# Kernel optimization log

Hardware: AMD Instinct MI355X
Metric: run time of the kernel (lower is better)

## Reference

```python
import jax, jax.numpy as jnp
import numpy as np

NUM_HEADS = 8
NUM_GROUPS = 8
EPS = 1e-5


def setup_inputs() -> dict:
    key = jax.random.key(0)
    ks = jax.random.split(key, 4)
    B, C, H, W = 16, 512, 32, 32
    x = jax.random.normal(ks[0], (B, C, H, W), dtype=jnp.float32)
    gamma = jnp.ones((C,), jnp.float32)
    beta = jnp.zeros((C,), jnp.float32)
    w_qkv = jax.random.normal(ks[1], (3 * C, C), jnp.float32) * (1.0 / np.sqrt(C))
    b_qkv = jnp.zeros((3 * C,), jnp.float32)
    w_out = jax.random.normal(ks[2], (C, C), jnp.float32) * (1.0 / np.sqrt(C))
    b_out = jnp.zeros((C,), jnp.float32)
    return {"x": x, "gamma": gamma, "beta": beta, "w_qkv": w_qkv,
            "b_qkv": b_qkv, "w_out": w_out, "b_out": b_out}


def _group_norm(x, gamma, beta):
    b, c, h, w = x.shape
    xg = x.reshape(b, NUM_GROUPS, c // NUM_GROUPS, h, w)
    mean = xg.mean(axis=(2, 3, 4), keepdims=True)
    var = xg.var(axis=(2, 3, 4), keepdims=True)
    xn = ((xg - mean) * jax.lax.rsqrt(var + EPS)).reshape(b, c, h, w)
    return xn * gamma[None, :, None, None] + beta[None, :, None, None]


def reference(x, gamma, beta, w_qkv, b_qkv, w_out, b_out):
    b, c, h, w = x.shape
    hd = c // NUM_HEADS
    scale = hd ** -0.5
    xn = _group_norm(x, gamma, beta)
    # 1x1 conv == per-pixel linear: (3c, c) x (b, c, h, w) -> (b, 3c, h, w)
    qkv = jnp.einsum('oc,bchw->bohw', w_qkv, xn) + b_qkv[None, :, None, None]
    q, k, v = jnp.split(qkv, 3, axis=1)
    q = q.reshape(b, NUM_HEADS, hd, h * w)
    k = k.reshape(b, NUM_HEADS, hd, h * w)
    v = v.reshape(b, NUM_HEADS, hd, h * w)
    attn = jnp.einsum('bhdi,bhdj->bhij', q, k) * scale  # (b, heads, hw, hw)
    attn = jax.nn.softmax(attn, axis=-1)
    out = jnp.einsum('bhij,bhdj->bhdi', attn, v).reshape(b, c, h, w)
    out = jnp.einsum('oc,bchw->bohw', w_out, out) + b_out[None, :, None, None]
    return x + out
```

## Files before the change

### kernel.cpp

```cpp
#include <hip/hip_runtime.h>
#include <hip/hip_bf16.h>

#define BB   16
#define CCH  512
#define PP   1024
#define NHD  8

typedef unsigned short u16;
typedef unsigned int   u32;
typedef __attribute__((ext_vector_type(8))) short bf16x8;
typedef __attribute__((ext_vector_type(4))) float f32x4;

__device__ __forceinline__ float us2f(u16 u) {
    return __uint_as_float(((u32)u) << 16);
}
__device__ __forceinline__ u16 f2bu(float f) {
    __hip_bfloat16 h = __float2bfloat16(f);
    return *reinterpret_cast<u16*>(&h);
}

__launch_bounds__(256)
__global__ void gn_stats_k(const float* __restrict__ x,
                           float* __restrict__ ps, float* __restrict__ pss) {
    int blk = blockIdx.x;
    int bg = blk >> 2, part = blk & 3;
    const float4* xp = (const float4*)(x + (size_t)bg * 65536 + (size_t)part * 16384);
    float s = 0.f, ss = 0.f;
    for (int i = threadIdx.x; i < 4096; i += 256) {
        float4 v = xp[i];
        s  += v.x + v.y + v.z + v.w;
        ss += v.x*v.x + v.y*v.y + v.z*v.z + v.w*v.w;
    }
    __shared__ float sh[256], sq[256];
    sh[threadIdx.x] = s; sq[threadIdx.x] = ss;
    __syncthreads();
    for (int off = 128; off > 0; off >>= 1) {
        if (threadIdx.x < off) {
            sh[threadIdx.x] += sh[threadIdx.x + off];
            sq[threadIdx.x] += sq[threadIdx.x + off];
        }
        __syncthreads();
    }
    if (threadIdx.x == 0) {
        ps[blk]  = sh[0];
        pss[blk] = sq[0];
    }
}

__launch_bounds__(256)
__global__ void conv_x_k(const float* __restrict__ x,
                         const float* __restrict__ ps, const float* __restrict__ pss,
                         const float* __restrict__ gamma, const float* __restrict__ beta,
                         u16* __restrict__ xbt) {
    __shared__ u16 T[64][73];
    const int tid = threadIdx.x;
    const int p0 = blockIdx.x * 64;
    const int c0 = blockIdx.y * 64;
    const int b  = blockIdx.z;
    const int bg = (b << 3) + (c0 >> 6);
    float s4  = ps[bg*4]  + ps[bg*4+1]  + ps[bg*4+2]  + ps[bg*4+3];
    float ss4 = pss[bg*4] + pss[bg*4+1] + pss[bg*4+2] + pss[bg*4+3];
    float m   = s4 * (1.f / 65536.f);
    float var = ss4 * (1.f / 65536.f) - m * m;
    float rs  = rsqrtf(var + 1e-5f);
    {
        int ci = tid >> 2, psx = (tid & 3) * 16;
        int c = c0 + ci;
        float sc = rs * gamma[c];
        float sf = beta[c] - m * sc;
        const float* xp = x + ((size_t)(b * CCH + c)) * PP + p0 + psx;
        #pragma unroll
        for (int j4 = 0; j4 < 4; j4++) {
            float4 v = *(const float4*)(xp + j4 * 4);
            T[psx + j4*4 + 0][ci] = f2bu(v.x * sc + sf);
            T[psx + j4*4 + 1][ci] = f2bu(v.y * sc + sf);
            T[psx + j4*4 + 2][ci] = f2bu(v.z * sc + sf);
            T[psx + j4*4 + 3][ci] = f2bu(v.w * sc + sf);
        }
    }
    __syncthreads();
    {
        int pi = tid >> 2, cs = (tid & 3) * 16;
        u16* dst = xbt + ((size_t)(b * PP) + p0 + pi) * CCH + c0 + cs;
        #pragma unroll
        for (int j4 = 0; j4 < 4; j4++) {
            ushort4 o;
            o.x = T[pi][cs + j4*4 + 0]; o.y = T[pi][cs + j4*4 + 1];
            o.z = T[pi][cs + j4*4 + 2]; o.w = T[pi][cs + j4*4 + 3];
            *(ushort4*)(dst + j4 * 4) = o;
        }
    }
}

__launch_bounds__(256)
__global__ void conv_w_k(const float* __restrict__ w1, const float* __restrict__ w2,
                         u16* __restrict__ d1, u16* __restrict__ d2) {
    int id = blockIdx.x * 256 + threadIdx.x;
    const float* s; u16* d; int off;
    if (id < 196608) { s = w1; d = d1; off = id * 4; }
    else             { s = w2; d = d2; off = (id - 196608) * 4; }
    float4 v = *(const float4*)(s + off);
    ushort4 o;
    o.x = f2bu(v.x); o.y = f2bu(v.y); o.z = f2bu(v.z); o.w = f2bu(v.w);
    *(ushort4*)(d + off) = o;
}

__launch_bounds__(256)
__global__ void mgemm_qkv_k(const u16* __restrict__ Wb, const float* __restrict__ bias,
                            const u16* __restrict__ actT,
                            u16* __restrict__ qT, u16* __restrict__ kT,
                            u16* __restrict__ v) {
    __shared__ __align__(16) u16 smem[17408];
    u16* As = smem;
    u16* Bs = smem + 5120;
    const int tid = threadIdx.x;
    const int p0 = blockIdx.x * 128;
    const int m0 = blockIdx.y * 128;
    const int b  = blockIdx.z;
    const int w = tid >> 6, l = tid & 63, quad = l >> 4, lm = l & 15;
    const int mo = (w >> 1) * 64, no = (w & 1) * 64;

    f32x4 acc[4][4] = {};

    const int srow = tid >> 1, sks = (tid & 1) << 4;
    const u16* wp = Wb + (size_t)(m0 + srow) * CCH + sks;
    const u16* ap = actT + (size_t)b * PP * CCH + (size_t)(p0 + srow) * CCH + sks;
    u16* asw = &As[srow * 40 + sks];
    u16* bsw = &Bs[srow * 40 + sks];

    uint4 aw0 = *(const uint4*)(wp);
    uint4 aw1 = *(const uint4*)(wp + 8);
    uint4 bw0 = *(const uint4*)(ap);
    uint4 bw1 = *(const uint4*)(ap + 8);

    for (int k0 = 0; k0 < CCH; k0 += 32) {
        *(uint4*)asw = aw0;  *(uint4*)(asw + 8) = aw1;
        *(uint4*)bsw = bw0;  *(uint4*)(bsw + 8) = bw1;
        __syncthreads();
        if (k0 + 32 < CCH) {
            aw0 = *(const uint4*)(wp + k0 + 32);
            aw1 = *(const uint4*)(wp + k0 + 40);
            bw0 = *(const uint4*)(ap + k0 + 32);
            bw1 = *(const uint4*)(ap + k0 + 40);
        }
        bf16x8 af[4], bfr[4];
        #pragma unroll
        for (int mi = 0; mi < 4; mi++)
            af[mi] = *(const bf16x8*)&As[(mo + mi*16 + lm) * 40 + quad * 8];
        #pragma unroll
        for (int ni = 0; ni < 4; ni++)
            bfr[ni] = *(const bf16x8*)&Bs[(no + ni*16 + lm) * 40 + quad * 8];
        __builtin_amdgcn_s_setprio(1);
        #pragma unroll
        for (int mi = 0; mi < 4; mi++)
            #pragma unroll
            for (int ni = 0; ni < 4; ni++)
                acc[mi][ni] = __builtin_amdgcn_mfma_f32_16x16x32_bf16(
                    af[mi], bfr[ni], acc[mi][ni], 0, 0, 0);
        __builtin_amdgcn_s_setprio(0);
        __syncthreads();
    }

    const int region = m0 >> 9;
    if (region < 2) {
        u16* Cb = smem;
        #pragma unroll
        for (int mi = 0; mi < 4; mi++) {
            f32x4 bv = *(const f32x4*)&bias[m0 + mo + mi*16 + quad*4];
            #pragma unroll
            for (int ni = 0; ni < 4; ni++) {
                int colp = no + ni*16 + lm;
                int rowb = mo + mi*16 + quad*4;
                #pragma unroll
                for (int r = 0; r < 4; r++)
                    Cb[colp * 136 + rowb + r] = f2bu(acc[mi][ni][r] + bv[r]);
            }
        }
        __syncthreads();
        int prow = tid >> 1, half = tid & 1;
        u16* base = (region == 0) ? qT : kT;
        u16* dst = base + ((size_t)b * PP + p0 + prow) * 512 + (m0 & 511) + half * 64;
        const u16* src = &Cb[prow * 136 + half * 64];
        #pragma unroll
        for (int i = 0; i < 8; i++)
            *(uint4*)(dst + i * 8) = *(const uint4*)(src + i * 8);
    } else {
        u16* Cb = smem;
        #pragma unroll
        for (int mi = 0; mi < 4; mi++) {
            f32x4 bv = *(const f32x4*)&bias[m0 + mo + mi*16 + quad*4];
            #pragma unroll
            for (int ni = 0; ni < 4; ni++) {
                int colp = no + ni*16 + lm;
                int rowb = mo + mi*16 + quad*4;
                #pragma unroll
                for (int r = 0; r < 4; r++)
                    Cb[(rowb + r) * 136 + colp] = f2bu(acc[mi][ni][r] + bv[r]);
            }
        }
        __syncthreads();
        int row = tid >> 1, half = tid & 1;
        u16* dst = v + ((size_t)b * 512 + (m0 - 1024) + row) * PP + p0 + half * 64;
        const u16* src = &Cb[row * 136 + half * 64];
        #pragma unroll
        for (int i = 0; i < 8; i++)
            *(uint4*)(dst + i * 8) = *(const uint4*)(src + i * 8);
    }
}

__launch_bounds__(512, 4)
__global__ void fattn_k(const u16* __restrict__ qT, const u16* __restrict__ kT,
                        const u16* __restrict__ v, u16* __restrict__ ao) {
    __shared__ __align__(16) u16 Ps[128 * 136];
    __shared__ __align__(16) u16 Ks[128 * 72];
    __shared__ __align__(16) u16 Vs[64 * 136];
    const int tid = threadIdx.x;
    const int q0 = blockIdx.x * 128;
    const int h  = blockIdx.y;
    const int b  = blockIdx.z;
    const int w = tid >> 6, l = tid & 63, quad = l >> 4, lm = l & 15;

    {
        int r = w * 16 + (l >> 2), c = (l & 3) * 16;
        const u16* src = qT + ((size_t)b * PP + q0 + r) * 512 + h * 64 + c;
        *(uint4*)&Ps[r * 136 + c]     = *(const uint4*)src;
        *(uint4*)&Ps[r * 136 + c + 8] = *(const uint4*)(src + 8);
    }
    bf16x8 qf0 = *(const bf16x8*)&Ps[(w * 16 + lm) * 136 + quad * 8];
    bf16x8 qf1 = *(const bf16x8*)&Ps[(w * 16 + lm) * 136 + 32 + quad * 8];

    f32x4 O[4] = {};
    float mrow[4] = {-3.0e38f, -3.0e38f, -3.0e38f, -3.0e38f};
    float lrow[4] = {};

    const int ksr = tid >> 2, ksc = (tid & 3) * 16;
    const int vsr = tid >> 3, vsc = (tid & 7) * 16;

    uint4 ka, kb, va, vb;
    {
        const u16* ksrc = kT + ((size_t)b * PP + ksr) * 512 + h * 64 + ksc;
        ka = *(const uint4*)ksrc; kb = *(const uint4*)(ksrc + 8);
        const u16* vsrc = v + ((size_t)b * 512 + h * 64 + vsr) * PP + vsc;
        va = *(const uint4*)vsrc; vb = *(const uint4*)(vsrc + 8);
    }

    for (int j0 = 0; j0 < PP; j0 += 128) {
        __syncthreads();
        *(uint4*)&Ks[ksr * 72 + ksc]      = ka;
        *(uint4*)&Ks[ksr * 72 + ksc + 8]  = kb;
        *(uint4*)&Vs[vsr * 136 + vsc]     = va;
        *(uint4*)&Vs[vsr * 136 + vsc + 8] = vb;
        __syncthreads();

        if (j0 + 128 < PP) {
            const u16* ksrc = kT + ((size_t)b * PP + j0 + 128 + ksr) * 512 + h * 64 + ksc;
            ka = *(const uint4*)ksrc; kb = *(const uint4*)(ksrc + 8);
            const u16* vsrc = v + ((size_t)b * 512 + h * 64 + vsr) * PP + j0 + 128 + vsc;
            va = *(const uint4*)vsrc; vb = *(const uint4*)(vsrc + 8);
        }

        f32x4 s[8];
        __builtin_amdgcn_s_setprio(1);
        #pragma unroll
        for (int ni = 0; ni < 8; ni++) {
            bf16x8 kf0 = *(const bf16x8*)&Ks[(ni*16 + lm) * 72 + quad * 8];
            bf16x8 kf1 = *(const bf16x8*)&Ks[(ni*16 + lm) * 72 + 32 + quad * 8];
            f32x4 z = {};
            z = __builtin_amdgcn_mfma_f32_16x16x32_bf16(qf0, kf0, z, 0, 0, 0);
            s[ni] = __builtin_amdgcn_mfma_f32_16x16x32_bf16(qf1, kf1, z, 0, 0, 0);
        }
        __builtin_amdgcn_s_setprio(0);

        #pragma unroll
        for (int r = 0; r < 4; r++) {
            float e[8];
            #pragma unroll
            for (int ni = 0; ni < 8; ni++) e[ni] = s[ni][r] * 0.18033688011f;
            float tm = fmaxf(fmaxf(fmaxf(e[0], e[1]), fmaxf(e[2], e[3])),
                             fmaxf(fmaxf(e[4], e[5]), fmaxf(e[6], e[7])));
            tm = fmaxf(tm, __shfl_xor(tm, 1));
            tm = fmaxf(tm, __shfl_xor(tm, 2));
            tm = fmaxf(tm, __shfl_xor(tm, 4));
            tm = fmaxf(tm, __shfl_xor(tm, 8));
            float mnew  = fmaxf(mrow[r], tm);
            float alpha = __builtin_amdgcn_exp2f(mrow[r] - mnew);
            mrow[r] = mnew;
            float ts = 0.f;
            int qq = (w * 16 + quad * 4 + r) * 136 + lm;
            #pragma unroll
            for (int ni = 0; ni < 8; ni++) {
                float p = __builtin_amdgcn_exp2f(e[ni] - mnew);
                ts += p;
                Ps[qq + ni * 16] = f2bu(p);
            }
            ts += __shfl_xor(ts, 1);
            ts += __shfl_xor(ts, 2);
            ts += __shfl_xor(ts, 4);
            ts += __shfl_xor(ts, 8);
            lrow[r] = lrow[r] * alpha + ts;
            O[0][r] *= alpha; O[1][r] *= alpha; O[2][r] *= alpha; O[3][r] *= alpha;
        }

        __builtin_amdgcn_s_setprio(1);
        #pragma unroll
        for (int kf = 0; kf < 4; kf++) {
            bf16x8 pf = *(const bf16x8*)&Ps[(w*16 + lm) * 136 + kf * 32 + quad * 8];
            #pragma unroll
            for (int nd = 0; nd < 4; nd++) {
                bf16x8 vf = *(const bf16x8*)&Vs[(nd*16 + lm) * 136 + kf * 32 + quad * 8];
                O[nd] = __builtin_amdgcn_mfma_f32_16x16x32_bf16(pf, vf, O[nd], 0, 0, 0);
            }
        }
        __builtin_amdgcn_s_setprio(0);
    }

    #pragma unroll
    for (int r = 0; r < 4; r++) {
        float rinv = 1.f / lrow[r];
        int qq = (w * 16 + quad * 4 + r) * 136 + lm;
        Ps[qq]      = f2bu(O[0][r] * rinv);
        Ps[qq + 16] = f2bu(O[1][r] * rinv);
        Ps[qq + 32] = f2bu(O[2][r] * rinv);
        Ps[qq + 48] = f2bu(O[3][r] * rinv);
    }
    {
        int r = w * 16 + (l >> 2), c = (l & 3) * 16;
        u16* dst = ao + ((size_t)b * PP + q0 + r) * 512 + h * 64 + c;
        *(uint4*)dst       = *(const uint4*)&Ps[r * 136 + c];
        *(uint4*)(dst + 8) = *(const uint4*)&Ps[r * 136 + c + 8];
    }
}

__launch_bounds__(256)
__global__ void mgemm_out_k(const u16* __restrict__ Wb, const float* __restrict__ bias,
                            const u16* __restrict__ actT, const float* __restrict__ resid,
                            float* __restrict__ out) {
    __shared__ __align__(16) u16 smem[10240];
    u16* As = smem;
    u16* Bs = smem + 5120;
    const int tid = threadIdx.x;
    const int p0 = blockIdx.x * 128;
    const int m0 = blockIdx.y * 128;
    const int b  = blockIdx.z;
    const int w = tid >> 6, l = tid & 63, quad = l >> 4, lm = l & 15;
    const int mo = (w >> 1) * 64, no = (w & 1) * 64;

    f32x4 acc[4][4] = {};

    const int srow = tid >> 1, sks = (tid & 1) << 4;
    const u16* wp = Wb + (size_t)(m0 + srow) * CCH + sks;
    const u16* ap = actT + (size_t)b * PP * CCH + (size_t)(p0 + srow) * CCH + sks;
    u16* asw = &As[srow * 40 + sks];
    u16* bsw = &Bs[srow * 40 + sks];

    uint4 aw0 = *(const uint4*)(wp);
    uint4 aw1 = *(const uint4*)(wp + 8);
    uint4 bw0 = *(const uint4*)(ap);
    uint4 bw1 = *(const uint4*)(ap + 8);

    for (int k0 = 0; k0 < CCH; k0 += 32) {
        *(uint4*)asw = aw0;  *(uint4*)(asw + 8) = aw1;
        *(uint4*)bsw = bw0;  *(uint4*)(bsw + 8) = bw1;
        __syncthreads();
        if (k0 + 32 < CCH) {
            aw0 = *(const uint4*)(wp + k0 + 32);
            aw1 = *(const uint4*)(wp + k0 + 40);
            bw0 = *(const uint4*)(ap + k0 + 32);
            bw1 = *(const uint4*)(ap + k0 + 40);
        }
        bf16x8 af[4], bfr[4];
        #pragma unroll
        for (int mi = 0; mi < 4; mi++)
            af[mi] = *(const bf16x8*)&As[(mo + mi*16 + lm) * 40 + quad * 8];
        #pragma unroll
        for (int ni = 0; ni < 4; ni++)
            bfr[ni] = *(const bf16x8*)&Bs[(no + ni*16 + lm) * 40 + quad * 8];
        __builtin_amdgcn_s_setprio(1);
        #pragma unroll
        for (int mi = 0; mi < 4; mi++)
            #pragma unroll
            for (int ni = 0; ni < 4; ni++)
                acc[mi][ni] = __builtin_amdgcn_mfma_f32_16x16x32_bf16(
                    af[mi], bfr[ni], acc[mi][ni], 0, 0, 0);
        __builtin_amdgcn_s_setprio(0);
        __syncthreads();
    }

    #pragma unroll
    for (int mi = 0; mi < 4; mi++) {
        f32x4 bv = *(const f32x4*)&bias[m0 + mo + mi*16 + quad*4];
        #pragma unroll
        for (int ni = 0; ni < 4; ni++) {
            int p = p0 + no + ni*16 + lm;
            #pragma unroll
            for (int r = 0; r < 4; r++) {
                int m = m0 + mo + mi*16 + quad*4 + r;
                size_t idx = ((size_t)b * CCH + m) * PP + p;
                out[idx] = acc[mi][ni][r] + bv[r] + resid[idx];
            }
        }
    }
}

extern "C" void kernel_launch(void* const* d_in, const int* in_sizes, int n_in,
                              void* d_out, int out_size, void* d_ws, size_t ws_size,
                              hipStream_t stream) {
    const float* x     = (const float*)d_in[0];
    const float* gamma = (const float*)d_in[1];
    const float* beta  = (const float*)d_in[2];
    const float* w_qkv = (const float*)d_in[3];
    const float* b_qkv = (const float*)d_in[4];
    const float* w_out = (const float*)d_in[5];
    const float* b_out = (const float*)d_in[6];

    char* ws = (char*)d_ws;
    float* ps  = (float*)ws;
    float* pss = (float*)(ws + 2048);
    u16* wqb = (u16*)(ws + 4096);
    u16* wob = wqb + 1536 * 512;
    u16* xbt = wob + 512 * 512;
    u16* ao  = xbt + (size_t)BB * PP * CCH;
    u16* qTb = ao  + (size_t)BB * PP * CCH;
    u16* kTb = qTb + (size_t)BB * PP * CCH;
    u16* vb  = kTb + (size_t)BB * PP * CCH;

    gn_stats_k<<<512, 256, 0, stream>>>(x, ps, pss);
    conv_x_k<<<dim3(16, 8, 16), 256, 0, stream>>>(x, ps, pss, gamma, beta, xbt);
    conv_w_k<<<1024, 256, 0, stream>>>(w_qkv, w_out, wqb, wob);
    mgemm_qkv_k<<<dim3(8, 12, 16), 256, 0, stream>>>(wqb, b_qkv, xbt, qTb, kTb, vb);
    fattn_k<<<dim3(8, 8, 16), 512, 0, stream>>>(qTb, kTb, vb, ao);
    mgemm_out_k<<<dim3(8, 4, 16), 256, 0, stream>>>(wob, b_out, ao, x, (float*)d_out);
}
```

Measured before the change: 264.3 us.

## Fuse pre-kernels, fold softmax scale into Q, MFMA row-sum, swizzle LDS, remap blocks

Merges the GroupNorm-stats and weight-conversion kernels into one launch, which saves a kernel launch. The softmax scale is folded into the Q projection epilogue, so the attention loop no longer multiplies every score. The per-row softmax sum is now computed by an extra MFMA against a vector of ones, which replaces the shuffle reductions. The P tile in LDS uses an XOR swizzle to reduce bank conflicts. Grids are flattened with a remapped block order that spreads work across XCDs for better L2 locality. The costs are an extra MFMA per k-fragment and a row sum taken over bf16-rounded probabilities.

Measured after the change: 250.3 us. -5.3%, faster.

```diff
diff --git a/kernel.cpp b/kernel.cpp
--- a/kernel.cpp
+++ b/kernel.cpp
@@ -11,39 +11,49 @@
 typedef __attribute__((ext_vector_type(8))) short bf16x8;
 typedef __attribute__((ext_vector_type(4))) float f32x4;
 
-__device__ __forceinline__ float us2f(u16 u) {
-    return __uint_as_float(((u32)u) << 16);
-}
 __device__ __forceinline__ u16 f2bu(float f) {
     __hip_bfloat16 h = __float2bfloat16(f);
     return *reinterpret_cast<u16*>(&h);
 }
 
 __launch_bounds__(256)
-__global__ void gn_stats_k(const float* __restrict__ x,
-                           float* __restrict__ ps, float* __restrict__ pss) {
+__global__ void pre_k(const float* __restrict__ x,
+                      float* __restrict__ ps, float* __restrict__ pss,
+                      const float* __restrict__ w1, const float* __restrict__ w2,
+                      u16* __restrict__ d1, u16* __restrict__ d2) {
     int blk = blockIdx.x;
-    int bg = blk >> 2, part = blk & 3;
-    const float4* xp = (const float4*)(x + (size_t)bg * 65536 + (size_t)part * 16384);
-    float s = 0.f, ss = 0.f;
-    for (int i = threadIdx.x; i < 4096; i += 256) {
-        float4 v = xp[i];
-        s  += v.x + v.y + v.z + v.w;
-        ss += v.x*v.x + v.y*v.y + v.z*v.z + v.w*v.w;
-    }
-    __shared__ float sh[256], sq[256];
-    sh[threadIdx.x] = s; sq[threadIdx.x] = ss;
-    __syncthreads();
-    for (int off = 128; off > 0; off >>= 1) {
-        if (threadIdx.x < off) {
-            sh[threadIdx.x] += sh[threadIdx.x + off];
-            sq[threadIdx.x] += sq[threadIdx.x + off];
-        }
-        __syncthreads();
-    }
-    if (threadIdx.x == 0) {
-        ps[blk]  = sh[0];
-        pss[blk] = sq[0];
+    if (blk < 512) {
+        int bg = blk >> 2, part = blk & 3;
+        const float4* xp = (const float4*)(x + (size_t)bg * 65536 + (size_t)part * 16384);
+        float s = 0.f, ss = 0.f;
+        for (int i = threadIdx.x; i < 4096; i += 256) {
+            float4 v = xp[i];
+            s  += v.x + v.y + v.z + v.w;
+            ss += v.x*v.x + v.y*v.y + v.z*v.z + v.w*v.w;
+        }
+        __shared__ float sh[256], sq[256];
+        sh[threadIdx.x] = s; sq[threadIdx.x] = ss;
+        __syncthreads();
+        for (int off = 128; off > 0; off >>= 1) {
+            if (threadIdx.x < off) {
+                sh[threadIdx.x] += sh[threadIdx.x + off];
+                sq[threadIdx.x] += sq[threadIdx.x + off];
+            }
+            __syncthreads();
+        }
+        if (threadIdx.x == 0) {
+            ps[blk]  = sh[0];
+            pss[blk] = sq[0];
+        }
+    } else {
+        int id = (blk - 512) * 256 + threadIdx.x;
+        const float* s; u16* d; int off;
+        if (id < 196608) { s = w1; d = d1; off = id * 4; }
+        else             { s = w2; d = d2; off = (id - 196608) * 4; }
+        float4 v = *(const float4*)(s + off);
+        ushort4 o;
+        o.x = f2bu(v.x); o.y = f2bu(v.y); o.z = f2bu(v.z); o.w = f2bu(v.w);
+        *(ushort4*)(d + off) = o;
     }
 }
 
@@ -93,19 +103,6 @@
 }
 
 __launch_bounds__(256)
-__global__ void conv_w_k(const float* __restrict__ w1, const float* __restrict__ w2,
-                         u16* __restrict__ d1, u16* __restrict__ d2) {
-    int id = blockIdx.x * 256 + threadIdx.x;
-    const float* s; u16* d; int off;
-    if (id < 196608) { s = w1; d = d1; off = id * 4; }
-    else             { s = w2; d = d2; off = (id - 196608) * 4; }
-    float4 v = *(const float4*)(s + off);
-    ushort4 o;
-    o.x = f2bu(v.x); o.y = f2bu(v.y); o.z = f2bu(v.z); o.w = f2bu(v.w);
-    *(ushort4*)(d + off) = o;
-}
-
-__launch_bounds__(256)
 __global__ void mgemm_qkv_k(const u16* __restrict__ Wb, const float* __restrict__ bias,
                             const u16* __restrict__ actT,
                             u16* __restrict__ qT, u16* __restrict__ kT,
@@ -114,9 +111,12 @@
     u16* As = smem;
     u16* Bs = smem + 5120;
     const int tid = threadIdx.x;
-    const int p0 = blockIdx.x * 128;
-    const int m0 = blockIdx.y * 128;
-    const int b  = blockIdx.z;
+    const int id = blockIdx.x;
+    const int wk = (id & 7) * 192 + (id >> 3);
+    const int b  = wk / 96;
+    const int wi = wk % 96;
+    const int m0 = (wi >> 3) * 128;
+    const int p0 = (wi & 7) * 128;
     const int w = tid >> 6, l = tid & 63, quad = l >> 4, lm = l & 15;
     const int mo = (w >> 1) * 64, no = (w & 1) * 64;
 
@@ -163,6 +163,7 @@
 
     const int region = m0 >> 9;
     if (region < 2) {
+        const float scl = (region == 0) ? 0.18033688011f : 1.0f;
         u16* Cb = smem;
         #pragma unroll
         for (int mi = 0; mi < 4; mi++) {
@@ -173,7 +174,7 @@
                 int rowb = mo + mi*16 + quad*4;
                 #pragma unroll
                 for (int r = 0; r < 4; r++)
-                    Cb[colp * 136 + rowb + r] = f2bu(acc[mi][ni][r] + bv[r]);
+                    Cb[colp * 136 + rowb + r] = f2bu((acc[mi][ni][r] + bv[r]) * scl);
             }
         }
         __syncthreads();
@@ -215,23 +216,32 @@
     __shared__ __align__(16) u16 Ks[128 * 72];
     __shared__ __align__(16) u16 Vs[64 * 136];
     const int tid = threadIdx.x;
-    const int q0 = blockIdx.x * 128;
-    const int h  = blockIdx.y;
-    const int b  = blockIdx.z;
+    const int id = blockIdx.x;
+    const int wk = ((id & 7) << 7) | (id >> 3);
+    const int q0 = (wk & 7) * 128;
+    const int pair = wk >> 3;
+    const int h = pair & 7;
+    const int b = pair >> 3;
     const int w = tid >> 6, l = tid & 63, quad = l >> 4, lm = l & 15;
+    const int psw = ((lm >> 2) & 3) << 4;
 
     {
         int r = w * 16 + (l >> 2), c = (l & 3) * 16;
+        int swz = ((l >> 4) & 3) << 4;
         const u16* src = qT + ((size_t)b * PP + q0 + r) * 512 + h * 64 + c;
-        *(uint4*)&Ps[r * 136 + c]     = *(const uint4*)src;
-        *(uint4*)&Ps[r * 136 + c + 8] = *(const uint4*)(src + 8);
-    }
-    bf16x8 qf0 = *(const bf16x8*)&Ps[(w * 16 + lm) * 136 + quad * 8];
-    bf16x8 qf1 = *(const bf16x8*)&Ps[(w * 16 + lm) * 136 + 32 + quad * 8];
+        *(uint4*)&Ps[r * 136 + (c ^ swz)]     = *(const uint4*)src;
+        *(uint4*)&Ps[r * 136 + (c ^ swz) + 8] = *(const uint4*)(src + 8);
+    }
+    bf16x8 qf0 = *(const bf16x8*)&Ps[(w * 16 + lm) * 136 + ((quad * 8) ^ psw)];
+    bf16x8 qf1 = *(const bf16x8*)&Ps[(w * 16 + lm) * 136 + ((32 + quad * 8) ^ psw)];
+
+    bf16x8 onesv;
+    #pragma unroll
+    for (int i = 0; i < 8; i++) onesv[i] = (short)0x3F80;
 
     f32x4 O[4] = {};
+    f32x4 Ol = {};
     float mrow[4] = {-3.0e38f, -3.0e38f, -3.0e38f, -3.0e38f};
-    float lrow[4] = {};
 
     const int ksr = tid >> 2, ksc = (tid & 3) * 16;
     const int vsr = tid >> 3, vsc = (tid & 7) * 16;
@@ -273,11 +283,8 @@
 
         #pragma unroll
         for (int r = 0; r < 4; r++) {
-            float e[8];
-            #pragma unroll
-            for (int ni = 0; ni < 8; ni++) e[ni] = s[ni][r] * 0.18033688011f;
-            float tm = fmaxf(fmaxf(fmaxf(e[0], e[1]), fmaxf(e[2], e[3])),
-                             fmaxf(fmaxf(e[4], e[5]), fmaxf(e[6], e[7])));
+            float tm = fmaxf(fmaxf(fmaxf(s[0][r], s[1][r]), fmaxf(s[2][r], s[3][r])),
+                             fmaxf(fmaxf(s[4][r], s[5][r]), fmaxf(s[6][r], s[7][r])));
             tm = fmaxf(tm, __shfl_xor(tm, 1));
             tm = fmaxf(tm, __shfl_xor(tm, 2));
             tm = fmaxf(tm, __shfl_xor(tm, 4));
@@ -285,26 +292,21 @@
             float mnew  = fmaxf(mrow[r], tm);
             float alpha = __builtin_amdgcn_exp2f(mrow[r] - mnew);
             mrow[r] = mnew;
-            float ts = 0.f;
-            int qq = (w * 16 + quad * 4 + r) * 136 + lm;
+            int rowb = (w * 16 + quad * 4 + r) * 136 + lm;
             #pragma unroll
             for (int ni = 0; ni < 8; ni++) {
-                float p = __builtin_amdgcn_exp2f(e[ni] - mnew);
-                ts += p;
-                Ps[qq + ni * 16] = f2bu(p);
-            }
-            ts += __shfl_xor(ts, 1);
-            ts += __shfl_xor(ts, 2);
-            ts += __shfl_xor(ts, 4);
-            ts += __shfl_xor(ts, 8);
-            lrow[r] = lrow[r] * alpha + ts;
+                float p = __builtin_amdgcn_exp2f(s[ni][r] - mnew);
+                Ps[rowb + 16 * (ni ^ quad)] = f2bu(p);
+            }
             O[0][r] *= alpha; O[1][r] *= alpha; O[2][r] *= alpha; O[3][r] *= alpha;
+            Ol[r] *= alpha;
         }
 
         __builtin_amdgcn_s_setprio(1);
         #pragma unroll
         for (int kf = 0; kf < 4; kf++) {
-            bf16x8 pf = *(const bf16x8*)&Ps[(w*16 + lm) * 136 + kf * 32 + quad * 8];
+            bf16x8 pf = *(const bf16x8*)&Ps[(w*16 + lm) * 136 + ((kf * 32 + quad * 8) ^ psw)];
+            Ol = __builtin_amdgcn_mfma_f32_16x16x32_bf16(pf, onesv, Ol, 0, 0, 0);
             #pragma unroll
             for (int nd = 0; nd < 4; nd++) {
                 bf16x8 vf = *(const bf16x8*)&Vs[(nd*16 + lm) * 136 + kf * 32 + quad * 8];
@@ -316,18 +318,19 @@
 
     #pragma unroll
     for (int r = 0; r < 4; r++) {
-        float rinv = 1.f / lrow[r];
-        int qq = (w * 16 + quad * 4 + r) * 136 + lm;
-        Ps[qq]      = f2bu(O[0][r] * rinv);
-        Ps[qq + 16] = f2bu(O[1][r] * rinv);
-        Ps[qq + 32] = f2bu(O[2][r] * rinv);
-        Ps[qq + 48] = f2bu(O[3][r] * rinv);
+        float rinv = 1.f / Ol[r];
+        int rowb = (w * 16 + quad * 4 + r) * 136 + lm;
+        Ps[rowb + 16 * (0 ^ quad)] = f2bu(O[0][r] * rinv);
+        Ps[rowb + 16 * (1 ^ quad)] = f2bu(O[1][r] * rinv);
+        Ps[rowb + 16 * (2 ^ quad)] = f2bu(O[2][r] * rinv);
+        Ps[rowb + 16 * (3 ^ quad)] = f2bu(O[3][r] * rinv);
     }
     {
         int r = w * 16 + (l >> 2), c = (l & 3) * 16;
+        int swz = ((l >> 4) & 3) << 4;
         u16* dst = ao + ((size_t)b * PP + q0 + r) * 512 + h * 64 + c;
-        *(uint4*)dst       = *(const uint4*)&Ps[r * 136 + c];
-        *(uint4*)(dst + 8) = *(const uint4*)&Ps[r * 136 + c + 8];
+        *(uint4*)dst       = *(const uint4*)&Ps[r * 136 + (c ^ swz)];
+        *(uint4*)(dst + 8) = *(const uint4*)&Ps[r * 136 + (c ^ swz) + 8];
     }
 }
 
@@ -339,9 +342,12 @@
     u16* As = smem;
     u16* Bs = smem + 5120;
     const int tid = threadIdx.x;
-    const int p0 = blockIdx.x * 128;
-    const int m0 = blockIdx.y * 128;
-    const int b  = blockIdx.z;
+    const int id = blockIdx.x;
+    const int wk = (id & 7) * 64 + (id >> 3);
+    const int b  = wk >> 5;
+    const int wi = wk & 31;
+    const int m0 = (wi >> 3) * 128;
+    const int p0 = (wi & 7) * 128;
     const int w = tid >> 6, l = tid & 63, quad = l >> 4, lm = l & 15;
     const int mo = (w >> 1) * 64, no = (w & 1) * 64;
 
@@ -424,10 +430,9 @@
     u16* kTb = qTb + (size_t)BB * PP * CCH;
     u16* vb  = kTb + (size_t)BB * PP * CCH;
 
-    gn_stats_k<<<512, 256, 0, stream>>>(x, ps, pss);
+    pre_k<<<1536, 256, 0, stream>>>(x, ps, pss, w_qkv, w_out, wqb, wob);
     conv_x_k<<<dim3(16, 8, 16), 256, 0, stream>>>(x, ps, pss, gamma, beta, xbt);
-    conv_w_k<<<1024, 256, 0, stream>>>(w_qkv, w_out, wqb, wob);
-    mgemm_qkv_k<<<dim3(8, 12, 16), 256, 0, stream>>>(wqb, b_qkv, xbt, qTb, kTb, vb);
-    fattn_k<<<dim3(8, 8, 16), 512, 0, stream>>>(qTb, kTb, vb, ao);
-    mgemm_out_k<<<dim3(8, 4, 16), 256, 0, stream>>>(wob, b_out, ao, x, (float*)d_out);
-}
+    mgemm_qkv_k<<<1536, 256, 0, stream>>>(wqb, b_qkv, xbt, qTb, kTb, vb);
+    fattn_k<<<1024, 512, 0, stream>>>(qTb, kTb, vb, ao);
+    mgemm_out_k<<<512, 256, 0, stream>>>(wob, b_out, ao, x, (float*)d_out);
+}
```
